# Kernel optimization log

Hardware: AMD Instinct MI355X
Metric: run time of the kernel (lower is better)

Reference implementation:

```python
import jax, jax.numpy as jnp
import numpy as np

HID = 4096
OUT = 4096
L = 64
R = 64
B = 4
S = 2048
QMAX = 7.0  # int4 symmetric range [-8, 7], scale uses 7


def _quantize_weight(key, out_f, in_f):
    # Mimics weight_quantizer.find_params + quantize(quantonly=True):
    # symmetric per-output-channel int4 quantization.
    w = jax.random.normal(key, (out_f, in_f), dtype=jnp.float32) * 0.02
    s = jnp.maximum(jnp.max(jnp.abs(w), axis=1) / QMAX, 1e-8)  # [out]
    wq = jnp.clip(jnp.round(w / s[:, None]), -8.0, 7.0).astype(jnp.int8)
    return wq, s


def setup_inputs() -> dict:
    key = jax.random.key(0)
    ks = jax.random.split(key, 8)
    # FlatQuant learned invertible transforms; use orthogonal init via QR
    ml = jnp.linalg.qr(jax.random.normal(ks[0], (L, L), dtype=jnp.float32))[0]
    mr = jnp.linalg.qr(jax.random.normal(ks[1], (R, R), dtype=jnp.float32))[0]
    wq, sq = _quantize_weight(ks[2], OUT, HID)
    wk, sk = _quantize_weight(ks[3], OUT, HID)
    wv, sv = _quantize_weight(ks[4], OUT, HID)
    hs = jax.random.normal(ks[5], (B, S, HID), dtype=jnp.float32)
    return {
        "hidden_states": hs,
        "left_trans": ml.T,  # module stores matrix_left.T
        "right_trans": mr,
        "wt_q": wq, "scale_q": sq,
        "wt_k": wk, "scale_k": sk,
        "wt_v": wv, "scale_v": sv,
    }


def _flat_quant_linear(x, left, right, w_int, w_scale):
    # AscendW4A4FlatQuantDynamicLinearMethod.apply:
    # 1) two-sided Kronecker transform on the hidden dim (H = L*R)
    # 2) dynamic per-token symmetric int4 activation quantization
    b, s, h = x.shape
    l = left.shape[0]
    r = right.shape[0]
    xr = x.reshape(b, s, l, r)
    xt = jnp.einsum('ml,bslr,rn->bsmn', left, xr, right).reshape(b, s, h)
    a_scale = jnp.maximum(jnp.max(jnp.abs(xt), axis=-1, keepdims=True) / QMAX, 1e-8)  # [b,s,1]
    xq = jnp.clip(jnp.round(xt / a_scale), -8.0, 7.0)
    y = jnp.einsum('bsh,oh->bso', xq, w_int.astype(jnp.float32))
    return y * a_scale * w_scale[None, None, :]


def reference(hidden_states, left_trans, right_trans, wt_q, scale_q, wt_k, scale_k, wt_v, scale_v):
    b, s, _ = hidden_states.shape
    pad = 0
    if (b % 16) and (s % 16):  # static shapes -> Python control flow is fine
        pad = (s // 16 + 1) * 16 - s
        hidden_states = jnp.pad(hidden_states, ((0, 0), (0, pad), (0, 0)))
    wq = wt_q.astype(jnp.int8) if wt_q.dtype != jnp.int8 else wt_q
    wk = wt_k.astype(jnp.int8) if wt_k.dtype != jnp.int8 else wt_k
    wv = wt_v.astype(jnp.int8) if wt_v.dtype != jnp.int8 else wt_v
    q = _flat_quant_linear(hidden_states, left_trans, right_trans, wq, scale_q)
    k = _flat_quant_linear(hidden_states, left_trans, right_trans, wk, scale_k)
    v = _flat_quant_linear(hidden_states, left_trans, right_trans, wv, scale_v)
    if pad:
        q, k, v = q[:, :s], k[:, :s], v[:, :s]
    return q, k, v
```

## Files before the change

### kernel.cpp

```cpp
#include <hip/hip_runtime.h>

#define HID   4096
#define OUTF  4096
#define NTOK  8192
#define PROJ_STRIDE 33554432ull

typedef int   i32x4 __attribute__((ext_vector_type(4)));
typedef float f32x4 __attribute__((ext_vector_type(4)));

__global__ __launch_bounds__(256) void cvt_weights_i8(const int* __restrict__ w,
                                                      char* __restrict__ o,
                                                      int n4) {
    int i = blockIdx.x * blockDim.x + threadIdx.x;
    if (i < n4) {
        int4 v = ((const int4*)w)[i];
        int packed = (v.x & 255) | ((v.y & 255) << 8) |
                     ((v.z & 255) << 16) | (v.w << 24);
        ((int*)o)[i] = packed;
    }
}

__global__ __launch_bounds__(256) void transpose64(const float* __restrict__ in,
                                                   float* __restrict__ out) {
    int i = blockIdx.x * 256 + threadIdx.x;
    int r = i >> 6, c = i & 63;
    out[c * 64 + r] = in[i];
}

__global__ __launch_bounds__(256) void transform_quant(
    const float* __restrict__ hs, const float* __restrict__ leftT,
    const float* __restrict__ right, char* __restrict__ xq,
    float* __restrict__ ascale) {
    __shared__ __align__(16) float Xs[4096];
    __shared__ __align__(16) float Ls[4096];
    __shared__ __align__(16) float Rs[4096];
    __shared__ float red[256];

    const int t   = blockIdx.x;
    const int tid = threadIdx.x;
    const int tm  = tid >> 4;
    const int tn  = tid & 15;

    {
        const float* src = hs + (size_t)t * HID;
        #pragma unroll
        for (int i = 0; i < 4; i++) {
            int c = tid + i * 256;
            __builtin_amdgcn_global_load_lds(
                (const __attribute__((address_space(1))) void*)(src + c * 4),
                (__attribute__((address_space(3))) void*)(Xs + c * 4), 16, 0, 0);
            __builtin_amdgcn_global_load_lds(
                (const __attribute__((address_space(1))) void*)(leftT + c * 4),
                (__attribute__((address_space(3))) void*)(Ls + c * 4), 16, 0, 0);
            __builtin_amdgcn_global_load_lds(
                (const __attribute__((address_space(1))) void*)(right + c * 4),
                (__attribute__((address_space(3))) void*)(Rs + c * 4), 16, 0, 0);
        }
    }
    __syncthreads();

    float acc[4][4];
    #pragma unroll
    for (int i = 0; i < 4; i++)
        #pragma unroll
        for (int j = 0; j < 4; j++) acc[i][j] = 0.f;

    #pragma unroll 4
    for (int l = 0; l < 64; l++) {
        f32x4 xv = *(const f32x4*)(Xs + l * 64 + tn * 4);
        f32x4 lv = *(const f32x4*)(Ls + l * 64 + tm * 4);
        #pragma unroll
        for (int i = 0; i < 4; i++)
            #pragma unroll
            for (int j = 0; j < 4; j++)
                acc[i][j] = fmaf(lv[i], xv[j], acc[i][j]);
    }
    __syncthreads();

    #pragma unroll
    for (int j = 0; j < 4; j++) {
        int r = tn * 4 + j;
        int q = tm ^ (r & 7);
        f32x4 col = {acc[0][j], acc[1][j], acc[2][j], acc[3][j]};
        *(f32x4*)(Xs + r * 64 + q * 4) = col;
    }
    __syncthreads();

    #pragma unroll
    for (int i = 0; i < 4; i++)
        #pragma unroll
        for (int j = 0; j < 4; j++) acc[i][j] = 0.f;
    #pragma unroll 4
    for (int r = 0; r < 64; r++) {
        f32x4 rv = *(const f32x4*)(Rs + r * 64 + tn * 4);
        int q = tm ^ (r & 7);
        f32x4 tv = *(const f32x4*)(Xs + r * 64 + q * 4);
        #pragma unroll
        for (int i = 0; i < 4; i++)
            #pragma unroll
            for (int j = 0; j < 4; j++)
                acc[i][j] = fmaf(tv[i], rv[j], acc[i][j]);
    }

    float mx = 0.f;
    #pragma unroll
    for (int i = 0; i < 4; i++)
        #pragma unroll
        for (int j = 0; j < 4; j++) mx = fmaxf(mx, fabsf(acc[i][j]));
    red[tid] = mx;
    __syncthreads();
    for (int s = 128; s > 0; s >>= 1) {
        if (tid < s) red[tid] = fmaxf(red[tid], red[tid + s]);
        __syncthreads();
    }
    float scale = fmaxf(red[0] * (1.0f / 7.0f), 1e-8f);

    char* dst = xq + (size_t)t * HID;
    #pragma unroll
    for (int i = 0; i < 4; i++) {
        int packed = 0;
        #pragma unroll
        for (int j = 0; j < 4; j++) {
            float q = rintf(acc[i][j] / scale);
            q = fminf(fmaxf(q, -8.f), 7.f);
            packed |= ((int)q & 255) << (8 * j);
        }
        *(int*)(dst + (tm * 4 + i) * 64 + tn * 4) = packed;
    }
    if (tid == 0) ascale[t] = scale;
}

#define BM 128
#define BN 128
#define BKI 64

__global__ __launch_bounds__(256) void gemm_qkv(
    const char* __restrict__ xq, const float* __restrict__ ascale,
    const char* __restrict__ w8, const float* __restrict__ sq,
    const float* __restrict__ sk, const float* __restrict__ sv,
    float* __restrict__ out) {
    __shared__ __align__(16) char As[BM * BKI];
    __shared__ __align__(16) char Bs[BN * BKI];

    const int tid  = threadIdx.x;
    const int lane = tid & 63;
    const int wave = tid >> 6;
    const int wr   = wave >> 1;
    const int wc   = wave & 1;
    const int ml   = lane & 15;
    const int kq   = lane >> 4;

    const int mb   = blockIdx.x;
    const int proj = blockIdx.y >> 5;
    const int nb   = blockIdx.y & 31;

    const char* wp = w8 + (size_t)proj * ((size_t)OUTF * HID);
    const float* wscale = (proj == 0) ? sq : ((proj == 1) ? sk : sv);

    const size_t rowA0 = (size_t)mb * BM;
    const size_t rowB0 = (size_t)nb * BN;

    i32x4 acc[4][4];
    #pragma unroll
    for (int i = 0; i < 4; i++)
        #pragma unroll
        for (int j = 0; j < 4; j++) {
            i32x4 z = {0, 0, 0, 0};
            acc[i][j] = z;
        }

    for (int k0 = 0; k0 < HID; k0 += BKI) {
        #pragma unroll
        for (int tch = 0; tch < 2; tch++) {
            int c   = tid + tch * 256;
            int row = c >> 2, kc = c & 3;
            const char* g = xq + (rowA0 + row) * HID + k0 + kc * 16;
            __builtin_amdgcn_global_load_lds(
                (const __attribute__((address_space(1))) void*)g,
                (__attribute__((address_space(3))) void*)(As + c * 16), 16, 0, 0);
        }
        #pragma unroll
        for (int tch = 0; tch < 2; tch++) {
            int c   = tid + tch * 256;
            int row = c >> 2, kc = c & 3;
            const char* g = wp + (rowB0 + row) * HID + k0 + kc * 16;
            __builtin_amdgcn_global_load_lds(
                (const __attribute__((address_space(1))) void*)g,
                (__attribute__((address_space(3))) void*)(Bs + c * 16), 16, 0, 0);
        }
        __syncthreads();

        i32x4 af[4], bfr[4];
        #pragma unroll
        for (int i = 0; i < 4; i++)
            af[i] = *(const i32x4*)(As + (wr * 64 + i * 16 + ml) * BKI + kq * 16);
        #pragma unroll
        for (int j = 0; j < 4; j++)
            bfr[j] = *(const i32x4*)(Bs + (wc * 64 + j * 16 + ml) * BKI + kq * 16);

        #pragma unroll
        for (int i = 0; i < 4; i++)
            #pragma unroll
            for (int j = 0; j < 4; j++)
                acc[i][j] = __builtin_amdgcn_mfma_i32_16x16x64_i8(
                    af[i], bfr[j], acc[i][j], 0, 0, 0);
        __syncthreads();
    }

    #pragma unroll
    for (int i = 0; i < 4; i++) {
        #pragma unroll
        for (int rg = 0; rg < 4; rg++) {
            int row  = mb * BM + wr * 64 + i * 16 + kq * 4 + rg;
            float as = ascale[row];
            #pragma unroll
            for (int j = 0; j < 4; j++) {
                int col = nb * BN + wc * 64 + j * 16 + ml;
                out[(size_t)proj * PROJ_STRIDE + (size_t)row * OUTF + col] =
                    (float)acc[i][j][rg] * as * wscale[col];
            }
        }
    }
}

extern "C" void kernel_launch(void* const* d_in, const int* in_sizes, int n_in,
                              void* d_out, int out_size, void* d_ws, size_t ws_size,
                              hipStream_t stream) {
    const float* hs    = (const float*)d_in[0];
    const float* left  = (const float*)d_in[1];
    const float* right = (const float*)d_in[2];
    const int*   wq    = (const int*)d_in[3];
    const float* sq    = (const float*)d_in[4];
    const int*   wk    = (const int*)d_in[5];
    const float* sk    = (const float*)d_in[6];
    const int*   wv    = (const int*)d_in[7];
    const float* sv    = (const float*)d_in[8];
    float* out = (float*)d_out;

    char*  xq8  = (char*)d_ws;
    float* ascl = (float*)((char*)d_ws + 33554432ull);
    char*  w8   = (char*)d_ws + 33587200ull;
    float* ltT  = (float*)((char*)d_ws + 83918848ull);

    const int nW = OUTF * HID;
    const int n4 = nW / 4;
    dim3 cblk(256), cgrd((n4 + 255) / 256);
    cvt_weights_i8<<<cgrd, cblk, 0, stream>>>(wq, w8 + 0ull * (size_t)nW, n4);
    cvt_weights_i8<<<cgrd, cblk, 0, stream>>>(wk, w8 + 1ull * (size_t)nW, n4);
    cvt_weights_i8<<<cgrd, cblk, 0, stream>>>(wv, w8 + 2ull * (size_t)nW, n4);

    transpose64<<<dim3(16), dim3(256), 0, stream>>>(left, ltT);

    transform_quant<<<dim3(NTOK), dim3(256), 0, stream>>>(hs, ltT, right, xq8, ascl);

    gemm_qkv<<<dim3(NTOK / BM, 3 * (OUTF / BN)), dim3(256), 0, stream>>>(
        xq8, ascl, w8, sq, sk, sv, out);
}
```

Baseline: 1.237 ms.

## Rework transform to one wave per token and double-buffer the int8 GEMM

Result: slower. 1.329 ms (+7.5%).

```diff
diff --git a/kernel.cpp b/kernel.cpp
--- a/kernel.cpp
+++ b/kernel.cpp
@@ -5,8 +5,9 @@
 #define NTOK  8192
 #define PROJ_STRIDE 33554432ull
 
-typedef int   i32x4 __attribute__((ext_vector_type(4)));
-typedef float f32x4 __attribute__((ext_vector_type(4)));
+typedef int   i32x4  __attribute__((ext_vector_type(4)));
+typedef int   i32x16 __attribute__((ext_vector_type(16)));
+typedef float f32x4  __attribute__((ext_vector_type(4)));
 
 __global__ __launch_bounds__(256) void cvt_weights_i8(const int* __restrict__ w,
                                                       char* __restrict__ o,
@@ -27,200 +28,222 @@
     out[c * 64 + r] = in[i];
 }
 
-__global__ __launch_bounds__(256) void transform_quant(
+__global__ __launch_bounds__(128) void transform_quant(
     const float* __restrict__ hs, const float* __restrict__ leftT,
     const float* __restrict__ right, char* __restrict__ xq,
     float* __restrict__ ascale) {
-    __shared__ __align__(16) float Xs[4096];
-    __shared__ __align__(16) float Ls[4096];
-    __shared__ __align__(16) float Rs[4096];
-    __shared__ float red[256];
-
-    const int t   = blockIdx.x;
-    const int tid = threadIdx.x;
-    const int tm  = tid >> 4;
-    const int tn  = tid & 15;
-
-    {
-        const float* src = hs + (size_t)t * HID;
-        #pragma unroll
-        for (int i = 0; i < 4; i++) {
-            int c = tid + i * 256;
-            __builtin_amdgcn_global_load_lds(
-                (const __attribute__((address_space(1))) void*)(src + c * 4),
-                (__attribute__((address_space(3))) void*)(Xs + c * 4), 16, 0, 0);
-            __builtin_amdgcn_global_load_lds(
-                (const __attribute__((address_space(1))) void*)(leftT + c * 4),
-                (__attribute__((address_space(3))) void*)(Ls + c * 4), 16, 0, 0);
-            __builtin_amdgcn_global_load_lds(
-                (const __attribute__((address_space(1))) void*)(right + c * 4),
-                (__attribute__((address_space(3))) void*)(Rs + c * 4), 16, 0, 0);
-        }
-    }
-    __syncthreads();
-
-    float acc[4][4];
-    #pragma unroll
-    for (int i = 0; i < 4; i++)
-        #pragma unroll
-        for (int j = 0; j < 4; j++) acc[i][j] = 0.f;
-
-    #pragma unroll 4
+    __shared__ __align__(16) float Xw[2][4096];
+
+    const int wv   = threadIdx.x >> 6;
+    const int lane = threadIdx.x & 63;
+    const int t    = blockIdx.x * 2 + wv;
+    const int tm   = lane >> 3;
+    const int tn   = lane & 7;
+
+    const float* X = hs + (size_t)t * HID;
+    float* Tw = &Xw[wv][0];
+
+    #pragma unroll
+    for (int k = 0; k < 16; k++) {
+        __builtin_amdgcn_global_load_lds(
+            (const __attribute__((address_space(1))) void*)(X + k * 256 + lane * 4),
+            (__attribute__((address_space(3))) void*)(Tw + k * 256 + lane * 4),
+            16, 0, 0);
+    }
+    asm volatile("s_waitcnt vmcnt(0)" ::: "memory");
+
+    float acc[8][8];
+    #pragma unroll
+    for (int i = 0; i < 8; i++)
+        #pragma unroll
+        for (int j = 0; j < 8; j++) acc[i][j] = 0.f;
+
+    #pragma unroll 2
     for (int l = 0; l < 64; l++) {
-        f32x4 xv = *(const f32x4*)(Xs + l * 64 + tn * 4);
-        f32x4 lv = *(const f32x4*)(Ls + l * 64 + tm * 4);
+        f32x4 x0 = *(const f32x4*)(Tw + l * 64 + tn * 8);
+        f32x4 x1 = *(const f32x4*)(Tw + l * 64 + tn * 8 + 4);
+        f32x4 l0 = *(const f32x4*)(leftT + l * 64 + tm * 8);
+        f32x4 l1 = *(const f32x4*)(leftT + l * 64 + tm * 8 + 4);
         #pragma unroll
         for (int i = 0; i < 4; i++)
             #pragma unroll
-            for (int j = 0; j < 4; j++)
-                acc[i][j] = fmaf(lv[i], xv[j], acc[i][j]);
-    }
-    __syncthreads();
-
-    #pragma unroll
-    for (int j = 0; j < 4; j++) {
-        int r = tn * 4 + j;
-        int q = tm ^ (r & 7);
-        f32x4 col = {acc[0][j], acc[1][j], acc[2][j], acc[3][j]};
-        *(f32x4*)(Xs + r * 64 + q * 4) = col;
-    }
-    __syncthreads();
-
-    #pragma unroll
-    for (int i = 0; i < 4; i++)
-        #pragma unroll
-        for (int j = 0; j < 4; j++) acc[i][j] = 0.f;
-    #pragma unroll 4
+            for (int j = 0; j < 4; j++) {
+                acc[i][j]         = fmaf(l0[i], x0[j], acc[i][j]);
+                acc[i][j + 4]     = fmaf(l0[i], x1[j], acc[i][j + 4]);
+                acc[i + 4][j]     = fmaf(l1[i], x0[j], acc[i + 4][j]);
+                acc[i + 4][j + 4] = fmaf(l1[i], x1[j], acc[i + 4][j + 4]);
+            }
+    }
+
+    #pragma unroll
+    for (int j = 0; j < 8; j++) {
+        const int r = tn * 8 + j;
+        f32x4 c0 = {acc[0][j], acc[1][j], acc[2][j], acc[3][j]};
+        f32x4 c1 = {acc[4][j], acc[5][j], acc[6][j], acc[7][j]};
+        *(f32x4*)(Tw + r * 64 + (((2 * tm + 0) ^ tn) << 2)) = c0;
+        *(f32x4*)(Tw + r * 64 + (((2 * tm + 1) ^ tn) << 2)) = c1;
+    }
+
+    #pragma unroll
+    for (int i = 0; i < 8; i++)
+        #pragma unroll
+        for (int j = 0; j < 8; j++) acc[i][j] = 0.f;
+
+    #pragma unroll 2
     for (int r = 0; r < 64; r++) {
-        f32x4 rv = *(const f32x4*)(Rs + r * 64 + tn * 4);
-        int q = tm ^ (r & 7);
-        f32x4 tv = *(const f32x4*)(Xs + r * 64 + q * 4);
+        f32x4 t0 = *(const f32x4*)(Tw + r * 64 + (((2 * tm + 0) ^ (r >> 3)) << 2));
+        f32x4 t1 = *(const f32x4*)(Tw + r * 64 + (((2 * tm + 1) ^ (r >> 3)) << 2));
+        f32x4 r0 = *(const f32x4*)(right + r * 64 + tn * 8);
+        f32x4 r1 = *(const f32x4*)(right + r * 64 + tn * 8 + 4);
         #pragma unroll
         for (int i = 0; i < 4; i++)
             #pragma unroll
-            for (int j = 0; j < 4; j++)
-                acc[i][j] = fmaf(tv[i], rv[j], acc[i][j]);
+            for (int j = 0; j < 4; j++) {
+                acc[i][j]         = fmaf(t0[i], r0[j], acc[i][j]);
+                acc[i][j + 4]     = fmaf(t0[i], r1[j], acc[i][j + 4]);
+                acc[i + 4][j]     = fmaf(t1[i], r0[j], acc[i + 4][j]);
+                acc[i + 4][j + 4] = fmaf(t1[i], r1[j], acc[i + 4][j + 4]);
+            }
     }
 
     float mx = 0.f;
     #pragma unroll
-    for (int i = 0; i < 4; i++)
-        #pragma unroll
-        for (int j = 0; j < 4; j++) mx = fmaxf(mx, fabsf(acc[i][j]));
-    red[tid] = mx;
-    __syncthreads();
-    for (int s = 128; s > 0; s >>= 1) {
-        if (tid < s) red[tid] = fmaxf(red[tid], red[tid + s]);
-        __syncthreads();
-    }
-    float scale = fmaxf(red[0] * (1.0f / 7.0f), 1e-8f);
+    for (int i = 0; i < 8; i++)
+        #pragma unroll
+        for (int j = 0; j < 8; j++) mx = fmaxf(mx, fabsf(acc[i][j]));
+    #pragma unroll
+    for (int d = 1; d < 64; d <<= 1) mx = fmaxf(mx, __shfl_xor(mx, d, 64));
+    const float scale = fmaxf(mx * (1.0f / 7.0f), 1e-8f);
 
     char* dst = xq + (size_t)t * HID;
     #pragma unroll
-    for (int i = 0; i < 4; i++) {
-        int packed = 0;
+    for (int i = 0; i < 8; i++) {
+        int p0 = 0, p1 = 0;
         #pragma unroll
         for (int j = 0; j < 4; j++) {
             float q = rintf(acc[i][j] / scale);
             q = fminf(fmaxf(q, -8.f), 7.f);
-            packed |= ((int)q & 255) << (8 * j);
-        }
-        *(int*)(dst + (tm * 4 + i) * 64 + tn * 4) = packed;
-    }
-    if (tid == 0) ascale[t] = scale;
-}
-
-#define BM 128
-#define BN 128
-#define BKI 64
-
-__global__ __launch_bounds__(256) void gemm_qkv(
+            p0 |= ((int)q & 255) << (8 * j);
+        }
+        #pragma unroll
+        for (int j = 4; j < 8; j++) {
+            float q = rintf(acc[i][j] / scale);
+            q = fminf(fmaxf(q, -8.f), 7.f);
+            p1 |= ((int)q & 255) << (8 * (j - 4));
+        }
+        *(int2*)(dst + (tm * 8 + i) * 64 + tn * 8) = make_int2(p0, p1);
+    }
+    if (lane == 0) ascale[t] = scale;
+}
+
+#define GBM 128
+#define GBK 128
+
+#define GSTAGE(BUF, KT)                                                       \
+  { _Pragma("unroll") for (int i_ = 0; i_ < 4; i_++) {                        \
+      const int c_ = tid + i_ * 256;                                          \
+      const int r_ = c_ >> 3;                                                 \
+      const int s_ = ((c_ ^ r_) & 7) << 4;                                    \
+      __builtin_amdgcn_global_load_lds(                                       \
+          (const __attribute__((address_space(1))) void*)                     \
+              (Ag + (size_t)r_ * HID + (KT) * GBK + s_),                      \
+          (__attribute__((address_space(3))) void*)                           \
+              (As + (BUF) * 16384 + c_ * 16), 16, 0, 0);                      \
+    }                                                                         \
+    _Pragma("unroll") for (int i_ = 0; i_ < 4; i_++) {                        \
+      const int c_ = tid + i_ * 256;                                          \
+      const int r_ = c_ >> 3;                                                 \
+      const int s_ = ((c_ ^ r_) & 7) << 4;                                    \
+      __builtin_amdgcn_global_load_lds(                                       \
+          (const __attribute__((address_space(1))) void*)                     \
+              (Bg + (size_t)r_ * HID + (KT) * GBK + s_),                      \
+          (__attribute__((address_space(3))) void*)                           \
+              (Bs + (BUF) * 16384 + c_ * 16), 16, 0, 0);                      \
+    }                                                                         \
+  }
+
+__global__ __launch_bounds__(256, 2) void gemm_qkv(
     const char* __restrict__ xq, const float* __restrict__ ascale,
     const char* __restrict__ w8, const float* __restrict__ sq,
     const float* __restrict__ sk, const float* __restrict__ sv,
     float* __restrict__ out) {
-    __shared__ __align__(16) char As[BM * BKI];
-    __shared__ __align__(16) char Bs[BN * BKI];
+    __shared__ __align__(16) char As[2 * 16384];
+    __shared__ __align__(16) char Bs[2 * 16384];
 
     const int tid  = threadIdx.x;
     const int lane = tid & 63;
     const int wave = tid >> 6;
     const int wr   = wave >> 1;
     const int wc   = wave & 1;
-    const int ml   = lane & 15;
-    const int kq   = lane >> 4;
-
-    const int mb   = blockIdx.x;
-    const int proj = blockIdx.y >> 5;
-    const int nb   = blockIdx.y & 31;
-
-    const char* wp = w8 + (size_t)proj * ((size_t)OUTF * HID);
+    const int l31  = lane & 31;
+    const int kh   = lane >> 5;
+    const int xk   = (l31 & 7) << 4;
+
+    const int wg   = blockIdx.x;
+    const int swz  = (wg & 7) * 768 + (wg >> 3);
+    const int proj = swz >> 11;
+    const int rr   = swz & 2047;
+    const int nb   = rr >> 6;
+    const int mb   = rr & 63;
+
+    const char* Ag = xq + (size_t)mb * GBM * HID;
+    const char* Bg = w8 + (size_t)proj * ((size_t)OUTF * HID) +
+                     (size_t)nb * GBM * HID;
     const float* wscale = (proj == 0) ? sq : ((proj == 1) ? sk : sv);
 
-    const size_t rowA0 = (size_t)mb * BM;
-    const size_t rowB0 = (size_t)nb * BN;
-
-    i32x4 acc[4][4];
-    #pragma unroll
-    for (int i = 0; i < 4; i++)
-        #pragma unroll
-        for (int j = 0; j < 4; j++) {
-            i32x4 z = {0, 0, 0, 0};
-            acc[i][j] = z;
-        }
-
-    for (int k0 = 0; k0 < HID; k0 += BKI) {
-        #pragma unroll
-        for (int tch = 0; tch < 2; tch++) {
-            int c   = tid + tch * 256;
-            int row = c >> 2, kc = c & 3;
-            const char* g = xq + (rowA0 + row) * HID + k0 + kc * 16;
-            __builtin_amdgcn_global_load_lds(
-                (const __attribute__((address_space(1))) void*)g,
-                (__attribute__((address_space(3))) void*)(As + c * 16), 16, 0, 0);
-        }
-        #pragma unroll
-        for (int tch = 0; tch < 2; tch++) {
-            int c   = tid + tch * 256;
-            int row = c >> 2, kc = c & 3;
-            const char* g = wp + (rowB0 + row) * HID + k0 + kc * 16;
-            __builtin_amdgcn_global_load_lds(
-                (const __attribute__((address_space(1))) void*)g,
-                (__attribute__((address_space(3))) void*)(Bs + c * 16), 16, 0, 0);
-        }
-        __syncthreads();
-
-        i32x4 af[4], bfr[4];
-        #pragma unroll
-        for (int i = 0; i < 4; i++)
-            af[i] = *(const i32x4*)(As + (wr * 64 + i * 16 + ml) * BKI + kq * 16);
-        #pragma unroll
-        for (int j = 0; j < 4; j++)
-            bfr[j] = *(const i32x4*)(Bs + (wc * 64 + j * 16 + ml) * BKI + kq * 16);
-
-        #pragma unroll
-        for (int i = 0; i < 4; i++)
-            #pragma unroll
-            for (int j = 0; j < 4; j++)
-                acc[i][j] = __builtin_amdgcn_mfma_i32_16x16x64_i8(
-                    af[i], bfr[j], acc[i][j], 0, 0, 0);
-        __syncthreads();
-    }
-
-    #pragma unroll
-    for (int i = 0; i < 4; i++) {
-        #pragma unroll
-        for (int rg = 0; rg < 4; rg++) {
-            int row  = mb * BM + wr * 64 + i * 16 + kq * 4 + rg;
-            float as = ascale[row];
-            #pragma unroll
-            for (int j = 0; j < 4; j++) {
-                int col = nb * BN + wc * 64 + j * 16 + ml;
+    i32x16 acc[2][2];
+    #pragma unroll
+    for (int i = 0; i < 2; i++)
+        #pragma unroll
+        for (int j = 0; j < 2; j++)
+            #pragma unroll
+            for (int e = 0; e < 16; e++) acc[i][j][e] = 0;
+
+    GSTAGE(0, 0);
+
+    for (int kt = 0; kt < 32; ++kt) {
+        const int cur = kt & 1;
+        if (kt < 31) {
+            GSTAGE(cur ^ 1, kt + 1);
+            asm volatile("s_waitcnt vmcnt(8)" ::: "memory");
+        } else {
+            asm volatile("s_waitcnt vmcnt(0)" ::: "memory");
+        }
+        __builtin_amdgcn_s_barrier();
+
+        const char* Ab = As + cur * 16384;
+        const char* Bb = Bs + cur * 16384;
+        __builtin_amdgcn_s_setprio(1);
+        #pragma unroll
+        for (int ks = 0; ks < 4; ks++) {
+            const int kb = ks * 32 + kh * 16;
+            i32x4 a0 = *(const i32x4*)(Ab + (wr * 64 + l31) * GBK + (kb ^ xk));
+            i32x4 a1 = *(const i32x4*)(Ab + (wr * 64 + 32 + l31) * GBK + (kb ^ xk));
+            i32x4 b0 = *(const i32x4*)(Bb + (wc * 64 + l31) * GBK + (kb ^ xk));
+            i32x4 b1 = *(const i32x4*)(Bb + (wc * 64 + 32 + l31) * GBK + (kb ^ xk));
+            acc[0][0] = __builtin_amdgcn_mfma_i32_32x32x32_i8(a0, b0, acc[0][0], 0, 0, 0);
+            acc[0][1] = __builtin_amdgcn_mfma_i32_32x32x32_i8(a0, b1, acc[0][1], 0, 0, 0);
+            acc[1][0] = __builtin_amdgcn_mfma_i32_32x32x32_i8(a1, b0, acc[1][0], 0, 0, 0);
+            acc[1][1] = __builtin_amdgcn_mfma_i32_32x32x32_i8(a1, b1, acc[1][1], 0, 0, 0);
+        }
+        __builtin_amdgcn_s_setprio(0);
+        __builtin_amdgcn_s_barrier();
+    }
+
+    const int rq = (lane >> 5) * 4;
+    #pragma unroll
+    for (int ib = 0; ib < 2; ib++)
+        #pragma unroll
+        for (int jb = 0; jb < 2; jb++) {
+            #pragma unroll
+            for (int reg = 0; reg < 16; reg++) {
+                const int rl  = (reg & 3) + 8 * (reg >> 2) + rq;
+                const int row = mb * GBM + wr * 64 + ib * 32 + rl;
+                const int col = nb * GBM + wc * 64 + jb * 32 + l31;
                 out[(size_t)proj * PROJ_STRIDE + (size_t)row * OUTF + col] =
-                    (float)acc[i][j][rg] * as * wscale[col];
+                    (float)acc[ib][jb][reg] * ascale[row] * wscale[col];
             }
         }
-    }
 }
 
 extern "C" void kernel_launch(void* const* d_in, const int* in_sizes, int n_in,
@@ -251,8 +274,8 @@
 
     transpose64<<<dim3(16), dim3(256), 0, stream>>>(left, ltT);
 
-    transform_quant<<<dim3(NTOK), dim3(256), 0, stream>>>(hs, ltT, right, xq8, ascl);
-
-    gemm_qkv<<<dim3(NTOK / BM, 3 * (OUTF / BN)), dim3(256), 0, stream>>>(
+    transform_quant<<<dim3(NTOK / 2), dim3(128), 0, stream>>>(hs, ltT, right, xq8, ascl);
+
+    gemm_qkv<<<dim3((NTOK / GBM) * (OUTF / GBM) * 3), dim3(256), 0, stream>>>(
         xq8, ascl, w8, sq, sk, sv, out);
 }
```
